# Kernel tuning notes

Measured on AMD Instinct MI355X. Metric: run time of the kernel, lower is better.

The kernel has to match this reference:

```python
import jax, jax.numpy as jnp
import numpy as np

B, M, D, DE = 2, 256, 256, 64  # batch, tokens, in_dim, dep_embed_dim


def setup_inputs() -> dict:
    key = jax.random.key(0)
    ks = jax.random.split(key, 10)
    features = jax.random.normal(ks[0], (B, M + 1, D), jnp.float32)
    dep_type_adj = jax.random.normal(ks[1], (B, M, M, DE), jnp.float32)
    adj = (jax.random.uniform(ks[2], (B, M, M)) < 0.05).astype(jnp.int32)
    idx = jnp.arange(M)
    adj = adj.at[:, idx, idx].set(1)
    asp_start = jax.random.randint(ks[3], (B,), 0, 200, dtype=jnp.int32)
    asp_end = asp_start + 16
    s = lambda fan_in: 1.0 / np.sqrt(fan_in)
    Wz = jax.random.normal(ks[4], (D, D), jnp.float32) * s(D)
    bz = jax.random.normal(ks[5], (D,), jnp.float32) * s(D)
    Wa = jax.random.normal(ks[6], (D + DE + D,), jnp.float32) * s(D + DE + D)
    Wm = jax.random.normal(ks[7], (D, D + DE), jnp.float32) * s(D + DE)
    Wh = jax.random.normal(ks[8], (D, 2 * D), jnp.float32) * s(2 * D)
    return dict(features=features, dep_type_adj=dep_type_adj, deprel_adj=adj,
                asp_start=asp_start, asp_end=asp_end,
                Wz=Wz, bz=bz, Wa=Wa, Wm=Wm, Wh=Wh)


def reference(features, dep_type_adj, deprel_adj, asp_start, asp_end, Wz, bz, Wa, Wm, Wh):
    # z_linear
    zf = features @ Wz.T + bz                              # [B, M+1, D]
    f = zf[:, 1:]                                          # token feats [B, M, D]
    asp = zf[0, 1:]                                        # NOTE: original indexes features[0] (batch 0)

    # candidate neighbors for node i: out-edges (i,j) then in-edges (j,i) -> 2M slots
    dep_cat = jnp.concatenate([dep_type_adj, jnp.swapaxes(dep_type_adj, 1, 2)], axis=2)  # [B,M,2M,DE]
    mask = jnp.concatenate([deprel_adj, jnp.swapaxes(deprel_adj, 1, 2)], axis=2) != 0    # [B,M,2M]

    # attention_layer weight split over [dep | neighbor_feat | aspect_feat]
    wa_dep, wa_nf, wa_asp = Wa[:DE], Wa[DE:DE + D], Wa[DE + D:]
    s = (jnp.einsum('bike,e->bik', dep_cat, wa_dep)
         + jnp.tile(f @ wa_nf, (1, 2))[:, None, :]
         + (asp @ wa_asp)[None, :, None])                  # [B,M,2M]
    s = jnp.where(s > 0, s, 0.01 * s)                      # LeakyReLU(0.01)
    big_neg = jnp.finfo(s.dtype).min
    w = jax.nn.softmax(jnp.where(mask, s, big_neg), axis=-1)
    w = jnp.where(mask, w, 0.0)                            # edge-softmax over valid neighbors

    # w_m over [dep | neighbor_feat]
    Wm_dep, Wm_f = Wm[:, :DE], Wm[:, DE:]
    nf_proj = jnp.tile(f @ Wm_f.T, (1, 2, 1))              # [B,2M,D], neighbor part (i-independent)
    msg = jax.nn.relu(jnp.einsum('bike,de->bikd', dep_cat, Wm_dep) + nf_proj[:, None])  # [B,M,2M,D]
    fused = jnp.einsum('bik,bikd->bid', w, msg)            # weighted aggregate [B,M,D]

    # w_h over [fused | aspect]
    out_asp = jax.nn.relu(fused @ Wh[:, :D].T + (asp @ Wh[:, D:].T)[None])  # [B,M,D]

    # only aspect-span nodes are updated; +1 offset into the token axis
    pos = jnp.arange(M)
    upd = (pos[None, :] >= asp_start[:, None]) & (pos[None, :] < asp_end[:, None])  # [B,M]
    tokens = jnp.where(upd[..., None], out_asp, features[:, 1:])
    return jnp.concatenate([features[:, :1], tokens], axis=1)  # dropout is identity at inference
```

## Files before the change

kernel.cpp:

```cpp
#include <hip/hip_runtime.h>
#include <hip/hip_bf16.h>
#include <cstdint>

#define BB 2
#define MM 256
#define DD 256
#define DE 64
#define K2 (2*MM)
#define WM_LD (DD+DE)
#define WH_LD (2*DD)
#define DEP_LD 68

__device__ float4 g_Wz4   [64*DD];
__device__ float4 g_Wm4   [64*DD];
__device__ float4 g_WmDep4[16*DD];
__device__ float4 g_Wh4lo [64*DD];
__device__ float4 g_Wh4hi [64*DD];
__device__ float g_fproj [BB*MM*DD];
__device__ float g_fnf   [BB*MM];
__device__ float g_aspdot[MM];
__device__ float g_asph  [MM*DD];

__global__ __launch_bounds__(256) void k_tr(const float* __restrict__ Wz,
                                            const float* __restrict__ Wm,
                                            const float* __restrict__ Wh,
                                            const float4* __restrict__ src,
                                            float4* __restrict__ dst, int n4) {
  const int t = threadIdx.x, blk = blockIdx.x;
  const int c = t & 63, r0 = t >> 6;
  __shared__ float tile[64][65];

  const int gidx = blk*256 + t;
  if (gidx < n4) dst[gidx] = src[gidx];

  const float* s = nullptr; float4* d4 = nullptr;
  int ld = 0, row0 = 0, col0 = 0, e4base = 0;
  if (blk < 16)      { s = Wz; ld = DD;    row0 = (blk>>2)*64; col0 = (blk&3)*64;      d4 = g_Wz4;    e4base = (blk&3)*16; }
  else if (blk < 32) { int x = blk-16; s = Wm; ld = WM_LD; row0 = (x>>2)*64; col0 = DE + (x&3)*64; d4 = g_Wm4; e4base = (x&3)*16; }
  else if (blk < 36) { int x = blk-32; s = Wm; ld = WM_LD; row0 = x*64;      col0 = 0;             d4 = g_WmDep4; e4base = 0; }
  else if (blk < 68) { int x = blk-36; int rt = x>>3, cg = x&7; s = Wh; ld = WH_LD; row0 = rt*64; col0 = cg*64;
                       d4 = (cg < 4) ? g_Wh4lo : g_Wh4hi; e4base = (cg&3)*16; }
  if (s) {
    #pragma unroll
    for (int rr = r0; rr < 64; rr += 4)
      tile[rr][c] = s[(size_t)(row0 + rr)*ld + col0 + c];
    __syncthreads();
    #pragma unroll
    for (int je = r0; je < 16; je += 4)
      d4[(size_t)(e4base + je)*DD + row0 + c] =
        make_float4(tile[c][4*je+0], tile[c][4*je+1], tile[c][4*je+2], tile[c][4*je+3]);
  }
}

__global__ __launch_bounds__(256) void k_pre(const float* __restrict__ feats,
                                             const float* __restrict__ bz,
                                             const float* __restrict__ Wa) {
  const int blk = blockIdx.x;
  const int b   = blk >> 7;
  const int m0  = (blk & 127) * 2;
  const int t   = threadIdx.x;

  __shared__ float fin[2][DD];
  __shared__ float fzsh[2][DD];

  fin[0][t] = feats[((size_t)b*(MM+1) + m0 + 1)*DD + t];
  fin[1][t] = feats[((size_t)b*(MM+1) + m0 + 2)*DD + t];
  __syncthreads();

  float a0 = 0.f, a1 = 0.f;
  #pragma unroll 8
  for (int e4 = 0; e4 < 64; ++e4) {
    const float4 w  = g_Wz4[(size_t)e4*DD + t];
    const float4 f0 = *(const float4*)&fin[0][e4*4];
    const float4 f1 = *(const float4*)&fin[1][e4*4];
    a0 += f0.x*w.x + f0.y*w.y + f0.z*w.z + f0.w*w.w;
    a1 += f1.x*w.x + f1.y*w.y + f1.z*w.z + f1.w*w.w;
  }
  const float bzt = bz[t];
  a0 += bzt; a1 += bzt;
  fzsh[0][t] = a0; fzsh[1][t] = a1;
  __syncthreads();

  const int wv = t >> 6, lane = t & 63;
  if (wv < 2) {
    float p = 0.f;
    for (int e = lane; e < DD; e += 64) p += fzsh[wv][e] * Wa[DE + e];
    for (int off = 32; off > 0; off >>= 1) p += __shfl_down(p, off, 64);
    if (lane == 0) g_fnf[b*MM + m0 + wv] = p;
  } else if (b == 0) {
    const int rr = wv - 2;
    float p = 0.f;
    for (int e = lane; e < DD; e += 64) p += fzsh[rr][e] * Wa[DE + DD + e];
    for (int off = 32; off > 0; off >>= 1) p += __shfl_down(p, off, 64);
    if (lane == 0) g_aspdot[m0 + rr] = p;
  }

  float p0 = 0.f, p1 = 0.f;
  #pragma unroll 8
  for (int e4 = 0; e4 < 64; ++e4) {
    const float4 w  = g_Wm4[(size_t)e4*DD + t];
    const float4 f0 = *(const float4*)&fzsh[0][e4*4];
    const float4 f1 = *(const float4*)&fzsh[1][e4*4];
    p0 += f0.x*w.x + f0.y*w.y + f0.z*w.z + f0.w*w.w;
    p1 += f1.x*w.x + f1.y*w.y + f1.z*w.z + f1.w*w.w;
  }
  g_fproj[((size_t)b*MM + m0    )*DD + t] = p0;
  g_fproj[((size_t)b*MM + m0 + 1)*DD + t] = p1;

  if (b == 0) {
    float q0 = 0.f, q1 = 0.f;
    #pragma unroll 8
    for (int e4 = 0; e4 < 64; ++e4) {
      const float4 w  = g_Wh4hi[(size_t)e4*DD + t];
      const float4 f0 = *(const float4*)&fzsh[0][e4*4];
      const float4 f1 = *(const float4*)&fzsh[1][e4*4];
      q0 += f0.x*w.x + f0.y*w.y + f0.z*w.z + f0.w*w.w;
      q1 += f1.x*w.x + f1.y*w.y + f1.z*w.z + f1.w*w.w;
    }
    g_asph[(size_t)(m0    )*DD + t] = q0;
    g_asph[(size_t)(m0 + 1)*DD + t] = q1;
  }
}

__global__ __launch_bounds__(256, 1) void k_attn(const float* __restrict__ dta,
                                                 const int*   __restrict__ adj,
                                                 const int*   __restrict__ a_start,
                                                 const int*   __restrict__ a_end,
                                                 const float* __restrict__ Wa,
                                                 float* __restrict__ out) {
  const int b = blockIdx.x >> 4;
  const int r = blockIdx.x & 15;
  const int i = a_start[b] + r;
  if (i >= a_end[b] || i >= MM) return;
  const int t = threadIdx.x;
  const int lane = t & 63, wv = t >> 6;
  const int d = t;

  __shared__ int   act[K2];
  __shared__ float sv [K2];
  __shared__ int   wcnt[8];
  __shared__ float wrm [4];
  __shared__ float wrs [4];
  __shared__ float wadep[DE];
  __shared__ float fnfsh[MM];
  __shared__ float depsh[64*DEP_LD];
  __shared__ float fproj_sh[64][DD];
  __shared__ float fused_sh[DD];

  const int mval0 = adj[((size_t)b*MM + i)*MM + t];
  const int mval1 = adj[((size_t)b*MM + t)*MM + i];
  float4 wm4[16];
  #pragma unroll
  for (int e4 = 0; e4 < 16; ++e4) wm4[e4] = g_WmDep4[(size_t)e4*DD + d];
  fnfsh[t] = g_fnf[b*MM + t];
  if (t < DE) wadep[t] = Wa[t];
  const float aspdot_i = g_aspdot[i];
  const float asph_i   = g_asph[(size_t)i*DD + d];

  const bool on0 = (mval0 != 0);
  const bool on1 = (mval1 != 0);
  const unsigned long long b0 = __ballot(on0);
  const unsigned long long b1 = __ballot(on1);
  if (lane == 0) { wcnt[wv] = __popcll(b0); wcnt[4+wv] = __popcll(b1); }
  __syncthreads();
  const int tot0 = wcnt[0] + wcnt[1] + wcnt[2] + wcnt[3];
  const int na   = tot0 + wcnt[4] + wcnt[5] + wcnt[6] + wcnt[7];
  {
    int off0 = 0, off1 = tot0;
    for (int w2 = 0; w2 < wv; ++w2) { off0 += wcnt[w2]; off1 += wcnt[4+w2]; }
    off0 += __popcll(b0 & ((1ull << lane) - 1ull));
    off1 += __popcll(b1 & ((1ull << lane) - 1ull));
    if (on0) act[off0] = t;
    if (on1) act[off1] = MM + t;
  }
  __syncthreads();

  const int jj = t >> 2, sub = t & 3;
  for (int base = 0; base < na; base += 64) {
    const int j = base + jj;
    float p = 0.f; int k = 0;
    if (j < na) {
      k = act[j];
      const float* dv = (k < MM) ? dta + (((size_t)b*MM + i)*MM + k)*DE
                                 : dta + (((size_t)b*MM + (k - MM))*MM + i)*DE;
      const float4* dv4 = (const float4*)dv + sub*4;
      const float4 v0 = dv4[0], v1 = dv4[1], v2 = dv4[2], v3 = dv4[3];
      const float* wa = wadep + sub*16;
      p = v0.x*wa[0]  + v0.y*wa[1]  + v0.z*wa[2]  + v0.w*wa[3]
        + v1.x*wa[4]  + v1.y*wa[5]  + v1.z*wa[6]  + v1.w*wa[7]
        + v2.x*wa[8]  + v2.y*wa[9]  + v2.z*wa[10] + v2.w*wa[11]
        + v3.x*wa[12] + v3.y*wa[13] + v3.z*wa[14] + v3.w*wa[15];
      if (base == 0) {
        float4* ds = (float4*)(depsh + jj*DEP_LD + sub*16);
        ds[0] = v0; ds[1] = v1; ds[2] = v2; ds[3] = v3;
      }
    }
    p += __shfl_xor(p, 1, 64);
    p += __shfl_xor(p, 2, 64);
    if (j < na && sub == 0) {
      const float s = p + fnfsh[k & (MM-1)] + aspdot_i;
      sv[j] = (s > 0.f) ? s : 0.01f * s;
    }
  }

  const int cnt0 = (na < 64) ? na : 64;
  const int nq0  = cnt0 * 64;
  float4 stash[16];
  #pragma unroll
  for (int rr = 0; rr < 16; ++rr) {
    const int q = t + rr*256;
    if (q < nq0) {
      const int jl = q >> 6, c4 = q & 63;
      const int k = act[jl];
      stash[rr] = *((const float4*)(g_fproj + ((size_t)b*MM + (k & (MM-1)))*DD) + c4);
    }
  }
  __syncthreads();

  {
    float part = -3.4e38f;
    for (int j = t; j < na; j += 256) part = fmaxf(part, sv[j]);
    for (int off = 32; off > 0; off >>= 1) part = fmaxf(part, __shfl_down(part, off, 64));
    if (lane == 0) wrm[wv] = part;
  }
  __syncthreads();
  const float mx = fmaxf(fmaxf(wrm[0], wrm[1]), fmaxf(wrm[2], wrm[3]));
  {
    float psum = 0.f;
    for (int j = t; j < na; j += 256) { float e = expf(sv[j] - mx); sv[j] = e; psum += e; }
    for (int off = 32; off > 0; off >>= 1) psum += __shfl_down(psum, off, 64);
    if (lane == 0) wrs[wv] = psum;
  }
  __syncthreads();
  const float inv = 1.f / (wrs[0] + wrs[1] + wrs[2] + wrs[3]);
  for (int j = t; j < na; j += 256) sv[j] *= inv;
  #pragma unroll
  for (int rr = 0; rr < 16; ++rr) {
    const int q = t + rr*256;
    if (q < nq0) { const int jl = q >> 6, c4 = q & 63; *(float4*)&fproj_sh[jl][c4*4] = stash[rr]; }
  }
  __syncthreads();

  float acc = 0.f;
  for (int base = 0; base < na; base += 64) {
    const int cnt = min(64, na - base);
    if (base > 0) {
      __syncthreads();
      for (int q = t; q < cnt*64; q += 256) {
        const int jl = q >> 6, c4 = q & 63;
        const int k = act[base + jl];
        *(float4*)&fproj_sh[jl][c4*4] =
          *((const float4*)(g_fproj + ((size_t)b*MM + (k & (MM-1)))*DD) + c4);
      }
      for (int q = t; q < cnt*16; q += 256) {
        const int jl = q >> 4, e4 = q & 15;
        const int k = act[base + jl];
        const float* dv = (k < MM) ? dta + (((size_t)b*MM + i)*MM + k)*DE
                                   : dta + (((size_t)b*MM + (k - MM))*MM + i)*DE;
        *(float4*)(depsh + jl*DEP_LD + e4*4) = ((const float4*)dv)[e4];
      }
      __syncthreads();
    }
    #pragma unroll 2
    for (int jl = 0; jl < cnt; ++jl) {
      const float4* dp = (const float4*)(depsh + jl*DEP_LD);
      float dot = 0.f;
      #pragma unroll
      for (int e4 = 0; e4 < 16; ++e4) {
        const float4 v = dp[e4];
        const float4 w = wm4[e4];
        dot += v.x*w.x + v.y*w.y + v.z*w.z + v.w*w.w;
      }
      float msg = dot + fproj_sh[jl][d];
      msg = (msg > 0.f) ? msg : 0.f;
      acc += sv[base + jl] * msg;
    }
  }
  fused_sh[d] = acc;
  __syncthreads();

  float o = asph_i;
  #pragma unroll 8
  for (int e4 = 0; e4 < 64; ++e4) {
    const float4 w = g_Wh4lo[(size_t)e4*DD + d];
    const float4 f = *(const float4*)&fused_sh[e4*4];
    o += f.x*w.x + f.y*w.y + f.z*w.z + f.w*w.w;
  }
  out[((size_t)b*(MM+1) + i + 1)*DD + d] = (o > 0.f) ? o : 0.f;
}

extern "C" void kernel_launch(void* const* d_in, const int* in_sizes, int n_in,
                              void* d_out, int out_size, void* d_ws, size_t ws_size,
                              hipStream_t stream) {
  const float* feats   = (const float*)d_in[0];
  const float* dta     = (const float*)d_in[1];
  const int*   adj     = (const int*)  d_in[2];
  const int*   a_start = (const int*)  d_in[3];
  const int*   a_end   = (const int*)  d_in[4];
  const float* Wz      = (const float*)d_in[5];
  const float* bz      = (const float*)d_in[6];
  const float* Wa      = (const float*)d_in[7];
  const float* Wm      = (const float*)d_in[8];
  const float* Wh      = (const float*)d_in[9];
  float* out = (float*)d_out;

  const int n4 = BB*(MM+1)*DD/4;
  k_tr  <<<132, 256, 0, stream>>>(Wz, Wm, Wh, (const float4*)feats, (float4*)out, n4);
  k_pre <<<BB*MM/2, 256, 0, stream>>>(feats, bz, Wa);
  k_attn<<<BB*16, 256, 0, stream>>>(dta, adj, a_start, a_end, Wa, out);
}
```

Baseline: 144.1 us.

## Process four rows per k_pre block and skip non-aspect asp projections

k_pre now handles four token rows per block instead of two, so each weight float4 load feeds four dot products and half as many blocks are launched. The aspect dot product and the Wh-hi projection for batch 0 are computed only for rows inside either batch's aspect span, skipping work whose results are never read. In k_attn the g_fproj stash loads are moved ahead of the score loop so they overlap it, and the message loop unroll goes from 2 to 4. The trade-off is fewer blocks for k_pre parallelism and more register pressure in both kernels.

```diff
diff --git a/kernel.cpp b/kernel.cpp
--- a/kernel.cpp
+++ b/kernel.cpp
@@ -54,71 +54,103 @@
 
 __global__ __launch_bounds__(256) void k_pre(const float* __restrict__ feats,
                                              const float* __restrict__ bz,
-                                             const float* __restrict__ Wa) {
+                                             const float* __restrict__ Wa,
+                                             const int*   __restrict__ a_start,
+                                             const int*   __restrict__ a_end) {
   const int blk = blockIdx.x;
-  const int b   = blk >> 7;
-  const int m0  = (blk & 127) * 2;
+  const int b   = blk >> 6;
+  const int m0  = (blk & 63) * 4;
   const int t   = threadIdx.x;
 
-  __shared__ float fin[2][DD];
-  __shared__ float fzsh[2][DD];
-
-  fin[0][t] = feats[((size_t)b*(MM+1) + m0 + 1)*DD + t];
-  fin[1][t] = feats[((size_t)b*(MM+1) + m0 + 2)*DD + t];
-  __syncthreads();
-
-  float a0 = 0.f, a1 = 0.f;
+  __shared__ float fin[4][DD];
+  __shared__ float fzsh[4][DD];
+
+  #pragma unroll
+  for (int r = 0; r < 4; ++r)
+    fin[r][t] = feats[((size_t)b*(MM+1) + m0 + r + 1)*DD + t];
+  __syncthreads();
+
+  float a0 = 0.f, a1 = 0.f, a2 = 0.f, a3 = 0.f;
   #pragma unroll 8
   for (int e4 = 0; e4 < 64; ++e4) {
     const float4 w  = g_Wz4[(size_t)e4*DD + t];
     const float4 f0 = *(const float4*)&fin[0][e4*4];
     const float4 f1 = *(const float4*)&fin[1][e4*4];
+    const float4 f2 = *(const float4*)&fin[2][e4*4];
+    const float4 f3 = *(const float4*)&fin[3][e4*4];
     a0 += f0.x*w.x + f0.y*w.y + f0.z*w.z + f0.w*w.w;
     a1 += f1.x*w.x + f1.y*w.y + f1.z*w.z + f1.w*w.w;
+    a2 += f2.x*w.x + f2.y*w.y + f2.z*w.z + f2.w*w.w;
+    a3 += f3.x*w.x + f3.y*w.y + f3.z*w.z + f3.w*w.w;
   }
   const float bzt = bz[t];
-  a0 += bzt; a1 += bzt;
-  fzsh[0][t] = a0; fzsh[1][t] = a1;
+  fzsh[0][t] = a0 + bzt; fzsh[1][t] = a1 + bzt;
+  fzsh[2][t] = a2 + bzt; fzsh[3][t] = a3 + bzt;
   __syncthreads();
 
   const int wv = t >> 6, lane = t & 63;
-  if (wv < 2) {
+  {
     float p = 0.f;
     for (int e = lane; e < DD; e += 64) p += fzsh[wv][e] * Wa[DE + e];
     for (int off = 32; off > 0; off >>= 1) p += __shfl_down(p, off, 64);
     if (lane == 0) g_fnf[b*MM + m0 + wv] = p;
-  } else if (b == 0) {
-    const int rr = wv - 2;
-    float p = 0.f;
-    for (int e = lane; e < DD; e += 64) p += fzsh[rr][e] * Wa[DE + DD + e];
-    for (int off = 32; off > 0; off >>= 1) p += __shfl_down(p, off, 64);
-    if (lane == 0) g_aspdot[m0 + rr] = p;
-  }
-
-  float p0 = 0.f, p1 = 0.f;
+  }
+  const int s0 = a_start[0], e0 = a_end[0], s1 = a_start[1], e1 = a_end[1];
+  if (b == 0) {
+    const int ri = m0 + wv;
+    if ((ri >= s0 && ri < e0) || (ri >= s1 && ri < e1)) {
+      float p = 0.f;
+      for (int e = lane; e < DD; e += 64) p += fzsh[wv][e] * Wa[DE + DD + e];
+      for (int off = 32; off > 0; off >>= 1) p += __shfl_down(p, off, 64);
+      if (lane == 0) g_aspdot[ri] = p;
+    }
+  }
+
+  float p0 = 0.f, p1 = 0.f, p2 = 0.f, p3 = 0.f;
   #pragma unroll 8
   for (int e4 = 0; e4 < 64; ++e4) {
     const float4 w  = g_Wm4[(size_t)e4*DD + t];
     const float4 f0 = *(const float4*)&fzsh[0][e4*4];
     const float4 f1 = *(const float4*)&fzsh[1][e4*4];
+    const float4 f2 = *(const float4*)&fzsh[2][e4*4];
+    const float4 f3 = *(const float4*)&fzsh[3][e4*4];
     p0 += f0.x*w.x + f0.y*w.y + f0.z*w.z + f0.w*w.w;
     p1 += f1.x*w.x + f1.y*w.y + f1.z*w.z + f1.w*w.w;
-  }
-  g_fproj[((size_t)b*MM + m0    )*DD + t] = p0;
+    p2 += f2.x*w.x + f2.y*w.y + f2.z*w.z + f2.w*w.w;
+    p3 += f3.x*w.x + f3.y*w.y + f3.z*w.z + f3.w*w.w;
+  }
+  g_fproj[((size_t)b*MM + m0 + 0)*DD + t] = p0;
   g_fproj[((size_t)b*MM + m0 + 1)*DD + t] = p1;
+  g_fproj[((size_t)b*MM + m0 + 2)*DD + t] = p2;
+  g_fproj[((size_t)b*MM + m0 + 3)*DD + t] = p3;
 
   if (b == 0) {
-    float q0 = 0.f, q1 = 0.f;
-    #pragma unroll 8
-    for (int e4 = 0; e4 < 64; ++e4) {
-      const float4 w  = g_Wh4hi[(size_t)e4*DD + t];
-      const float4 f0 = *(const float4*)&fzsh[0][e4*4];
-      const float4 f1 = *(const float4*)&fzsh[1][e4*4];
-      q0 += f0.x*w.x + f0.y*w.y + f0.z*w.z + f0.w*w.w;
-      q1 += f1.x*w.x + f1.y*w.y + f1.z*w.z + f1.w*w.w;
-    }
-    g_asph[(size_t)(m0    )*DD + t] = q0;
-    g_asph[(size_t)(m0 + 1)*DD + t] = q1;
+    bool need[4]; bool any = false;
+    #pragma unroll
+    for (int r = 0; r < 4; ++r) {
+      const int ri = m0 + r;
+      need[r] = ((ri >= s0 && ri < e0) || (ri >= s1 && ri < e1));
+      any = any || need[r];
+    }
+    if (any) {
+      float q0 = 0.f, q1 = 0.f, q2 = 0.f, q3 = 0.f;
+      #pragma unroll 8
+      for (int e4 = 0; e4 < 64; ++e4) {
+        const float4 w  = g_Wh4hi[(size_t)e4*DD + t];
+        const float4 f0 = *(const float4*)&fzsh[0][e4*4];
+        const float4 f1 = *(const float4*)&fzsh[1][e4*4];
+        const float4 f2 = *(const float4*)&fzsh[2][e4*4];
+        const float4 f3 = *(const float4*)&fzsh[3][e4*4];
+        q0 += f0.x*w.x + f0.y*w.y + f0.z*w.z + f0.w*w.w;
+        q1 += f1.x*w.x + f1.y*w.y + f1.z*w.z + f1.w*w.w;
+        q2 += f2.x*w.x + f2.y*w.y + f2.z*w.z + f2.w*w.w;
+        q3 += f3.x*w.x + f3.y*w.y + f3.z*w.z + f3.w*w.w;
+      }
+      if (need[0]) g_asph[(size_t)(m0+0)*DD + t] = q0;
+      if (need[1]) g_asph[(size_t)(m0+1)*DD + t] = q1;
+      if (need[2]) g_asph[(size_t)(m0+2)*DD + t] = q2;
+      if (need[3]) g_asph[(size_t)(m0+3)*DD + t] = q3;
+    }
   }
 }
 
@@ -174,6 +206,19 @@
     if (on1) act[off1] = MM + t;
   }
   __syncthreads();
+
+  const int cnt0 = (na < 64) ? na : 64;
+  const int nq0  = cnt0 * 64;
+  float4 stash[16];
+  #pragma unroll
+  for (int rr = 0; rr < 16; ++rr) {
+    const int q = t + rr*256;
+    if (q < nq0) {
+      const int jl = q >> 6, c4 = q & 63;
+      const int k = act[jl];
+      stash[rr] = *((const float4*)(g_fproj + ((size_t)b*MM + (k & (MM-1)))*DD) + c4);
+    }
+  }
 
   const int jj = t >> 2, sub = t & 3;
   for (int base = 0; base < na; base += 64) {
@@ -202,19 +247,6 @@
       sv[j] = (s > 0.f) ? s : 0.01f * s;
     }
   }
-
-  const int cnt0 = (na < 64) ? na : 64;
-  const int nq0  = cnt0 * 64;
-  float4 stash[16];
-  #pragma unroll
-  for (int rr = 0; rr < 16; ++rr) {
-    const int q = t + rr*256;
-    if (q < nq0) {
-      const int jl = q >> 6, c4 = q & 63;
-      const int k = act[jl];
-      stash[rr] = *((const float4*)(g_fproj + ((size_t)b*MM + (k & (MM-1)))*DD) + c4);
-    }
-  }
   __syncthreads();
 
   {
@@ -261,7 +293,7 @@
       }
       __syncthreads();
     }
-    #pragma unroll 2
+    #pragma unroll 4
     for (int jl = 0; jl < cnt; ++jl) {
       const float4* dp = (const float4*)(depsh + jl*DEP_LD);
       float dot = 0.f;
@@ -306,6 +338,6 @@
 
   const int n4 = BB*(MM+1)*DD/4;
   k_tr  <<<132, 256, 0, stream>>>(Wz, Wm, Wh, (const float4*)feats, (float4*)out, n4);
-  k_pre <<<BB*MM/2, 256, 0, stream>>>(feats, bz, Wa);
+  k_pre <<<BB*MM/4, 256, 0, stream>>>(feats, bz, Wa, a_start, a_end);
   k_attn<<<BB*16, 256, 0, stream>>>(dta, adj, a_start, a_end, Wa, out);
 }
```

Measured after the change: 169.8 us. 1.18x slower.
